# Optimization experiments

Hardware: AMD Instinct MI355X
Metric: run time of the kernel (lower is better)

## Reference

```python
import jax, jax.numpy as jnp
import numpy as np

B, O, I, D = 8, 128, 128, 1024


def setup_inputs() -> dict:
    key = jax.random.key(0)
    ks = jax.random.split(key, 10)
    s = 1.0 / np.sqrt(2 * D)  # torch Linear default-ish scale
    return {
        "output": jax.random.normal(ks[0], (B, O, D), jnp.float32),
        "context": jax.random.normal(ks[1], (B, I, D), jnp.float32),
        "mask": jax.random.randint(ks[2], (B, I), 0, 2, jnp.int32),
        # self.w = Linear(2*dim, dim), split into the output-half and context-half
        "w_out_w": jax.random.normal(ks[3], (D, D), jnp.float32) * s,
        "w_ctx_w": jax.random.normal(ks[4], (D, D), jnp.float32) * s,
        "w_b": jax.random.normal(ks[5], (D,), jnp.float32) * s,
        # self.score = Linear(dim, 1)
        "score_w": jax.random.normal(ks[6], (D,), jnp.float32) * (1.0 / np.sqrt(D)),
        "score_b": jnp.zeros((), jnp.float32),
        # self.linear_out = Linear(2*dim, dim)
        "lin_w": jax.random.normal(ks[7], (2 * D, D), jnp.float32) * s,
        "lin_b": jax.random.normal(ks[8], (D,), jnp.float32) * s,
    }


def reference(output, context, mask, w_out_w, w_ctx_w, w_b, score_w, score_b, lin_w, lin_b):
    # Additive (Bahdanau) attention.
    # cat(out, ctx) @ W^T == out @ W1 + ctx @ W2  -> avoid [B,O,I,2D] concat.
    s_out = jnp.einsum('bod,de->boe', output, w_out_w)            # [B,O,D]
    s_ctx = jnp.einsum('bid,de->bie', context, w_ctx_w)           # [B,I,D]
    h = jax.nn.leaky_relu(s_out[:, :, None, :] + s_ctx[:, None, :, :] + w_b)  # [B,O,I,D]
    score = jnp.einsum('boid,d->boi', h, score_w) + score_b       # [B,O,I]
    score = jnp.where(mask[:, None, :] == 1, -jnp.inf, score)
    attn = jax.nn.softmax(score, axis=-1)                         # [B,O,I]
    attn_output = jnp.einsum('boi,bid->bod', attn, context)       # mix=True: bmm
    # fn=True: linear_out on cat(attn_output, output) then leaky_relu
    combined = jnp.concatenate([attn_output, output], axis=-1)    # [B,O,2D]
    attn_output = jax.nn.leaky_relu(combined @ lin_w + lin_b)     # [B,O,D]
    return attn_output, attn
```

## Files before the change

### kernel.cpp

```cpp
#include <hip/hip_runtime.h>

namespace {

constexpr int kB = 8, kO = 128, kI = 128, kD = 1024;
constexpr long kOutAttnOff = (long)kB * kO * kD;

typedef __attribute__((ext_vector_type(8))) short short8;
typedef __attribute__((ext_vector_type(4))) float f32x4;

__device__ __forceinline__ float leaky(float x) { return fmaxf(x, 0.01f * x); }

__device__ __forceinline__ short f2bf(float f) {
    unsigned u = __builtin_bit_cast(unsigned, f);
    u += 0x7FFFu + ((u >> 16) & 1u);
    return (short)(u >> 16);
}

__device__ __forceinline__ void b8tof(const short8 v, float* f) {
    const unsigned* u = (const unsigned*)&v;
#pragma unroll
    for (int j = 0; j < 4; ++j) {
        f[2 * j]     = __builtin_bit_cast(float, u[j] << 16);
        f[2 * j + 1] = __builtin_bit_cast(float, u[j] & 0xffff0000u);
    }
}

__device__ __forceinline__ void gll16(const void* g, void* l) {
    __builtin_amdgcn_global_load_lds(
        (const __attribute__((address_space(1))) int*)g,
        (__attribute__((address_space(3))) int*)l, 16, 0, 0);
}

__global__ __launch_bounds__(256)
void conv_all(const float* __restrict__ output, const float* __restrict__ context,
              const float* __restrict__ w1, const float* __restrict__ w2,
              const float* __restrict__ lin,
              short* __restrict__ ob16, short* __restrict__ cb16,
              short* __restrict__ w1t, short* __restrict__ w2t,
              short* __restrict__ lint)
{
    __shared__ float T[64][68];
    const int bid = blockIdx.x, tid = threadIdx.x;

    if (bid < 1024) {
        const int idx = bid * 256 + tid;
        const float* src; short* dst; int i;
        if (idx < (1 << 17)) { src = output;  dst = ob16; i = idx; }
        else                 { src = context; dst = cb16; i = idx - (1 << 17); }
        const float4* s4 = (const float4*)src + (long)i * 2;
        const float4 v0 = s4[0], v1 = s4[1];
        short8 r;
        r[0] = f2bf(v0.x); r[1] = f2bf(v0.y); r[2] = f2bf(v0.z); r[3] = f2bf(v0.w);
        r[4] = f2bf(v1.x); r[5] = f2bf(v1.y); r[6] = f2bf(v1.z); r[7] = f2bf(v1.w);
        *(short8*)(dst + (long)i * 8) = r;
        return;
    }

    const int tb = bid - 1024;
    const float* src; short* dst; long C, R; int t2;
    if (tb < 256)      { src = w1;  dst = w1t;  R = 1024; C = 1024; t2 = tb; }
    else if (tb < 512) { src = w2;  dst = w2t;  R = 1024; C = 1024; t2 = tb - 256; }
    else               { src = lin; dst = lint; R = 2048; C = 1024; t2 = tb - 512; }
    const int tr = t2 >> 4, tc = t2 & 15;
    const int r = tid >> 2, q = tid & 3;

    const float* s = src + (long)(tr * 64 + r) * C + tc * 64 + q * 16;
    const float4 a0 = ((const float4*)s)[0];
    const float4 a1 = ((const float4*)s)[1];
    const float4 a2 = ((const float4*)s)[2];
    const float4 a3 = ((const float4*)s)[3];
    *(float4*)&T[r][q * 16 + 0]  = a0;
    *(float4*)&T[r][q * 16 + 4]  = a1;
    *(float4*)&T[r][q * 16 + 8]  = a2;
    *(float4*)&T[r][q * 16 + 12] = a3;
    __syncthreads();

    short8 o0, o1;
#pragma unroll
    for (int j = 0; j < 8; ++j)  o0[j] = f2bf(T[q * 16 + j][r]);
#pragma unroll
    for (int j = 0; j < 8; ++j)  o1[j] = f2bf(T[q * 16 + 8 + j][r]);
    short* dp = dst + (long)(tc * 64 + r) * R + tr * 64 + q * 16;
    *(short8*)dp       = o0;
    *((short8*)dp + 1) = o1;
}

__global__ __launch_bounds__(256)
void mm_jobs(const short* __restrict__ ob16, const short* __restrict__ cb16,
             const short* __restrict__ w1t, const short* __restrict__ w2t,
             const short* __restrict__ lint,
             const float* __restrict__ w_b, const float* __restrict__ lin_b,
             float* __restrict__ s_out, short* __restrict__ s_ctx16,
             float* __restrict__ outlin, short* __restrict__ ctxlin)
{
    __shared__ short As[2][64][64];
    __shared__ short Bs[2][128][64];
    const int tid = threadIdx.x;
    const int t = blockIdx.x;
    const int lane = tid & 63, w = tid >> 6;

    const short *Ap, *Bp;
    int lda, ldb, bm, bn, ldc;
    const float* bias = nullptr;
    float* Cf = nullptr;
    short* Ch = nullptr;

    if (t < 384) {
        const int job = t >> 7, jt = t & 127;
        bm = (jt >> 3) * 64; bn = (jt & 7) * 128;
        lda = 1024; ldc = 1024;
        if (job == 0)      { Ap = ob16; Bp = w1t;         ldb = 1024; bias = w_b;   Cf = s_out;   }
        else if (job == 1) { Ap = cb16; Bp = w2t;         ldb = 1024;               Ch = s_ctx16; }
        else               { Ap = ob16; Bp = lint + 1024; ldb = 2048; bias = lin_b; Cf = outlin;  }
    } else {
        const int tt = t - 384, bz = tt >> 4, tw = tt & 15;
        bm = tw * 64; bn = 0;
        Ap = lint; lda = 2048;
        Bp = cb16 + (long)bz * (kI * kD); ldb = 1024;
        Ch = ctxlin + (long)bz * (kD * kI); ldc = 128;
    }

    const int m0 = (w >> 1) * 32, n0 = (w & 1) * 64;
    const int fr = lane & 15, fcol = lane >> 4, sl = lane & 7;
    const int r8 = lane >> 3;
    const int sw8 = ((lane & 7) ^ r8) * 8;
    const int w16 = w * 16, w32 = w * 32;

    f32x4 acc[2][4] = {};

    auto stage = [&](int buf, int k0) {
        const short* ga = Ap + (long)(bm + w16 + r8) * lda + k0 + sw8;
        gll16(ga,                 &As[buf][w16][0]);
        gll16(ga + 8 * (long)lda, &As[buf][w16 + 8][0]);
        const short* gb = Bp + (long)(bn + w32 + r8) * ldb + k0 + sw8;
        gll16(gb,                  &Bs[buf][w32][0]);
        gll16(gb + 8 * (long)ldb,  &Bs[buf][w32 + 8][0]);
        gll16(gb + 16 * (long)ldb, &Bs[buf][w32 + 16][0]);
        gll16(gb + 24 * (long)ldb, &Bs[buf][w32 + 24][0]);
    };

    stage(0, 0);
    __syncthreads();
    int cur = 0;
    for (int s = 0; s < 16; ++s) {
        if (s < 15) stage(cur ^ 1, (s + 1) << 6);
#pragma unroll
        for (int ks8 = 0; ks8 < 8; ks8 += 4) {
            const int sa = ((ks8 + fcol) ^ sl) * 8;
            short8 a[2], b[4];
#pragma unroll
            for (int mi = 0; mi < 2; ++mi)
                a[mi] = *(const short8*)&As[cur][m0 + mi * 16 + fr][sa];
#pragma unroll
            for (int ni = 0; ni < 4; ++ni)
                b[ni] = *(const short8*)&Bs[cur][n0 + ni * 16 + fr][sa];
#pragma unroll
            for (int mi = 0; mi < 2; ++mi)
#pragma unroll
                for (int ni = 0; ni < 4; ++ni)
                    acc[mi][ni] = __builtin_amdgcn_mfma_f32_16x16x32_bf16(
                        a[mi], b[ni], acc[mi][ni], 0, 0, 0);
        }
        __syncthreads();
        cur ^= 1;
    }

    float bv[4] = {0, 0, 0, 0};
    if (bias) {
#pragma unroll
        for (int ni = 0; ni < 4; ++ni) bv[ni] = bias[bn + n0 + ni * 16 + fr];
    }
#pragma unroll
    for (int mi = 0; mi < 2; ++mi)
#pragma unroll
        for (int ni = 0; ni < 4; ++ni)
#pragma unroll
            for (int r = 0; r < 4; ++r) {
                const int row = bm + m0 + mi * 16 + ((lane >> 4) << 2) + r;
                const int col = bn + n0 + ni * 16 + fr;
                float v = acc[mi][ni][r] + bv[ni];
                if (Ch) Ch[(long)row * ldc + col] = f2bf(v);
                else    Cf[(long)row * ldc + col] = v;
            }
}

__global__ __launch_bounds__(256)
void score_final(const float* __restrict__ s_out, const short* __restrict__ s_ctx16,
                 const float* __restrict__ score_w, const float* __restrict__ score_b,
                 const int* __restrict__ mask, const short* __restrict__ ctxlin,
                 const float* __restrict__ outlin, float* __restrict__ out_main,
                 float* __restrict__ attn_f32)
{
    __shared__ float As[2][1032];
    __shared__ __align__(16) char CsPool[32768];
    __shared__ float Wsh[1024];
    __shared__ float Ps[4][2][128];
    __shared__ float Psi[4][128];
    __shared__ float so_sh[2];
    __shared__ int   Msk[128];
    __shared__ __align__(16) short Pl[16][136];

    short* CsS = (short*)CsPool;
    const int b   = blockIdx.x;
    const int o0  = blockIdx.y * 2;
    const int tid = threadIdx.x;
    const int wv  = tid >> 6;
    const int ln  = tid & 63;
    const int fr  = ln & 15, fg = ln >> 4;

    const float* arow = s_out + (long)(b * kO + o0) * kD;
#pragma unroll
    for (int q = 0; q < 2; ++q) {
        const int tq = tid + q * 256;
        const int rr = tq >> 8, c4 = (tq & 255) * 4;
        *(float4*)&As[rr][c4] = *(const float4*)&arow[(long)rr * kD + c4];
    }
    *(float4*)&Wsh[tid * 4] = *(const float4*)&score_w[tid * 4];
    if (tid < 128) Msk[tid] = mask[b * kI + tid];
    {
        short* pf = &Pl[0][0];
        for (int j = tid; j < 272; j += 256) *(short8*)(pf + j * 8) = short8{};
    }

    const short* crow = s_ctx16 + (long)b * kI * kD;
    auto stageCs = [&](int buf, int dc) {
#pragma unroll
        for (int it = 0; it < 4; ++it) {
            const int rb = wv * 32 + it * 8;
            const int r  = rb + (ln >> 3);
            const int sc = (ln & 7) ^ (r & 7);
            gll16(crow + (long)r * kD + dc + sc * 8, CsS + buf * 8192 + rb * 64);
        }
    };

    stageCs(0, 0);
    __syncthreads();

    if (wv < 2) {
        float acc = 0.0f;
#pragma unroll
        for (int j = 0; j < 16; j += 4) {
            const float4 av = *(const float4*)&As[wv][ln * 16 + j];
            const float4 ww = *(const float4*)&Wsh[ln * 16 + j];
            acc = fmaf(av.x, ww.x, acc); acc = fmaf(av.y, ww.y, acc);
            acc = fmaf(av.z, ww.z, acc); acc = fmaf(av.w, ww.w, acc);
        }
#pragma unroll
        for (int d = 1; d < 64; d <<= 1) acc += __shfl_xor(acc, d, 64);
        if (ln == 0) so_sh[wv] = acc;
    }

    float sa0[2] = {}, sa1[2] = {};
    float si0 = 0.0f, si1 = 0.0f;
    const int kb = wv * 16;

    int buf = 0;
    for (int c = 0; c < 16; ++c) {
        const int dc = c * 64;
        if (c < 15) stageCs(buf ^ 1, dc + 64);
        const int sc0 = ((wv * 2 + 0) ^ (ln & 7)) * 8;
        const int sc1 = ((wv * 2 + 1) ^ (ln & 7)) * 8;
        const short8 cA0 = *(const short8*)&CsS[buf * 8192 + ln * 64 + sc0];
        const short8 cA1 = *(const short8*)&CsS[buf * 8192 + ln * 64 + sc1];
        const short8 cB0 = *(const short8*)&CsS[buf * 8192 + (ln + 64) * 64 + sc0];
        const short8 cB1 = *(const short8*)&CsS[buf * 8192 + (ln + 64) * 64 + sc1];
        float c0[16], c1[16];
        b8tof(cA0, c0); b8tof(cA1, c0 + 8);
        b8tof(cB0, c1); b8tof(cB1, c1 + 8);
        float wr[16], av[2][16];
#pragma unroll
        for (int q = 0; q < 4; ++q) {
            *(float4*)&wr[q * 4]    = *(const float4*)&Wsh[dc + kb + q * 4];
            *(float4*)&av[0][q * 4] = *(const float4*)&As[0][dc + kb + q * 4];
            *(float4*)&av[1][q * 4] = *(const float4*)&As[1][dc + kb + q * 4];
        }
#pragma unroll
        for (int d = 0; d < 16; ++d) {
            si0 = fmaf(c0[d], wr[d], si0);
            si1 = fmaf(c1[d], wr[d], si1);
#pragma unroll
            for (int o = 0; o < 2; ++o) {
                sa0[o] = fmaf(__builtin_fabsf(av[o][d] + c0[d]), wr[d], sa0[o]);
                sa1[o] = fmaf(__builtin_fabsf(av[o][d] + c1[d]), wr[d], sa1[o]);
            }
        }
        __syncthreads();
        buf ^= 1;
    }

    short* Bsh = (short*)CsPool;
    const short* ctxb = ctxlin + (long)b * (kD * kI);
    auto stageB = [&](int half, int nc) {
#pragma unroll
        for (int it = 0; it < 4; ++it) {
            const int rb = wv * 16 + it * 4;
            const int r  = rb + (ln >> 4);
            const int n  = nc * 64 + r;
            const int sc = (ln & 15) ^ (r & 7);
            gll16(ctxb + (long)n * kI + sc * 8, Bsh + half * 8192 + rb * kI);
        }
    };
    stageB(0, 0);

#pragma unroll
    for (int o = 0; o < 2; ++o) {
        Ps[wv][o][ln]      = (o == 0) ? sa0[0] : sa0[1];
        Ps[wv][o][ln + 64] = (o == 0) ? sa1[0] : sa1[1];
    }
    Psi[wv][ln]      = si0;
    Psi[wv][ln + 64] = si1;
    __syncthreads();

    if (wv < 2) {
        const int ow = wv;
        const float negInf = -__builtin_huge_valf();
        const float sb = score_b[0];
        const float siT0 = Psi[0][ln] + Psi[1][ln] + Psi[2][ln] + Psi[3][ln];
        const float siT1 = Psi[0][ln + 64] + Psi[1][ln + 64]
                         + Psi[2][ln + 64] + Psi[3][ln + 64];
        const float saT0 = Ps[0][ow][ln] + Ps[1][ow][ln]
                         + Ps[2][ow][ln] + Ps[3][ow][ln];
        const float saT1 = Ps[0][ow][ln + 64] + Ps[1][ow][ln + 64]
                         + Ps[2][ow][ln + 64] + Ps[3][ow][ln + 64];
        const float soV = so_sh[ow];
        float s0 = 0.505f * (soV + siT0) + 0.495f * saT0 + sb;
        float s1 = 0.505f * (soV + siT1) + 0.495f * saT1 + sb;
        if (Msk[ln]      != 0) s0 = negInf;
        if (Msk[ln + 64] != 0) s1 = negInf;

        float m = fmaxf(s0, s1);
#pragma unroll
        for (int d = 1; d < 64; d <<= 1) m = fmaxf(m, __shfl_xor(m, d, 64));
        const float e0 = __expf(s0 - m);
        const float e1 = __expf(s1 - m);
        float sum = e0 + e1;
#pragma unroll
        for (int d = 1; d < 64; d <<= 1) sum += __shfl_xor(sum, d, 64);
        const float inv = 1.0f / sum;

        const long rowoff = (long)(b * kO + o0 + ow) * kI;
        const float p0 = e0 * inv, p1 = e1 * inv;
        attn_f32[rowoff + ln]      = p0;
        attn_f32[rowoff + ln + 64] = p1;
        Pl[ow][ln]      = f2bf(p0);
        Pl[ow][ln + 64] = f2bf(p1);
    }
    __syncthreads();

    int half = 0;
    for (int nc = 0; nc < 16; ++nc) {
        if (nc < 15) stageB(half ^ 1, nc + 1);
        const short* Bc = Bsh + half * 8192;
        f32x4 acc{};
#pragma unroll
        for (int ks = 0; ks < 4; ++ks) {
            const short8 a = *(const short8*)&Pl[fr][ks * 32 + fg * 8];
            const int sc = ((ks * 4 + fg) ^ (fr & 7)) * 8;
            const short8 bb = *(const short8*)&Bc[(wv * 16 + fr) * kI + sc];
            acc = __builtin_amdgcn_mfma_f32_16x16x32_bf16(a, bb, acc, 0, 0, 0);
        }
        if (fg == 0) {
#pragma unroll
            for (int r = 0; r < 2; ++r) {
                const int n = nc * 64 + wv * 16 + fr;
                const long off = (long)(b * kO + o0 + r) * kD + n;
                out_main[off] = leaky(acc[r] + outlin[off]);
            }
        }
        __syncthreads();
        half ^= 1;
    }
}

}

extern "C" void kernel_launch(void* const* d_in, const int* in_sizes, int n_in,
                              void* d_out, int out_size, void* d_ws, size_t ws_size,
                              hipStream_t stream)
{
    const float* output  = (const float*)d_in[0];
    const float* context = (const float*)d_in[1];
    const int*   mask    = (const int*)d_in[2];
    const float* w_out_w = (const float*)d_in[3];
    const float* w_ctx_w = (const float*)d_in[4];
    const float* w_b     = (const float*)d_in[5];
    const float* score_w = (const float*)d_in[6];
    const float* score_b = (const float*)d_in[7];
    const float* lin_w   = (const float*)d_in[8];
    const float* lin_b   = (const float*)d_in[9];

    float* out_main = (float*)d_out;
    float* out_attn = out_main + kOutAttnOff;
    float* s_out    = out_main;

    char* wp = (char*)d_ws;
    short* s_ctx16 = (short*)wp;  wp += (size_t)2 << 20;
    short* ob16    = (short*)wp;  wp += (size_t)2 << 20;
    short* cb16    = (short*)wp;  wp += (size_t)2 << 20;
    short* w1t     = (short*)wp;  wp += (size_t)2 << 20;
    short* w2t     = (short*)wp;  wp += (size_t)2 << 20;
    short* lint    = (short*)wp;  wp += (size_t)4 << 20;
    float* outlin  = (float*)wp;  wp += (size_t)4 << 20;
    short* ctxlin  = (short*)wp;

    const dim3 blk(256);

    hipLaunchKernelGGL(conv_all, dim3(2048), blk, 0, stream,
        output, context, w_out_w, w_ctx_w, lin_w, ob16, cb16, w1t, w2t, lint);

    hipLaunchKernelGGL(mm_jobs, dim3(512), blk, 0, stream,
        ob16, cb16, w1t, w2t, lint, w_b, lin_b, s_out, s_ctx16, outlin, ctxlin);

    hipLaunchKernelGGL(score_final, dim3(8, 64), blk, 0, stream,
        s_out, s_ctx16, score_w, score_b, mask, ctxlin, outlin, out_main, out_attn);
}
```

Before: 64.56 us.

## Triple-buffer LDS staging with explicit vmcnt waits in GEMM and score kernels

Replaces double-buffered global_load_lds staging with a three-slot ring in mm_jobs, the score loop and the final bmm loop of score_final. Two tiles are prefetched ahead, and the full __syncthreads is swapped for partial s_waitcnt vmcnt waits plus a raw s_barrier. The aim is to keep more global loads in flight and cut barrier and latency stalls between k-steps. In exchange it uses more LDS per block, which may lower occupancy. The hand-written vmcnt counts also depend on the exact order of other global memory operations in flight.

```diff
diff --git a/kernel.cpp b/kernel.cpp
--- a/kernel.cpp
+++ b/kernel.cpp
@@ -30,6 +30,12 @@
         (const __attribute__((address_space(1))) int*)g,
         (__attribute__((address_space(3))) int*)l, 16, 0, 0);
 }
+
+#define VMWAIT4() asm volatile("s_waitcnt vmcnt(4)" ::: "memory")
+#define VMWAIT6() asm volatile("s_waitcnt vmcnt(6)" ::: "memory")
+#define VMWAIT0() asm volatile("s_waitcnt vmcnt(0)" ::: "memory")
+#define LGKM0()   asm volatile("s_waitcnt lgkmcnt(0)" ::: "memory")
+#define BAR()     __builtin_amdgcn_s_barrier()
 
 __global__ __launch_bounds__(256)
 void conv_all(const float* __restrict__ output, const float* __restrict__ context,
@@ -93,8 +99,8 @@
              float* __restrict__ s_out, short* __restrict__ s_ctx16,
              float* __restrict__ outlin, short* __restrict__ ctxlin)
 {
-    __shared__ short As[2][64][64];
-    __shared__ short Bs[2][128][64];
+    __shared__ short As[3][64][64];
+    __shared__ short Bs[3][128][64];
     const int tid = threadIdx.x;
     const int t = blockIdx.x;
     const int lane = tid & 63, w = tid >> 6;
@@ -140,10 +146,13 @@
     };
 
     stage(0, 0);
-    __syncthreads();
-    int cur = 0;
+    stage(1, 64);
+    VMWAIT6();
+    BAR();
+
+    int cur = 0, s2 = 2;
     for (int s = 0; s < 16; ++s) {
-        if (s < 15) stage(cur ^ 1, (s + 1) << 6);
+        if (s + 2 < 16) stage(s2, (s + 2) << 6);
 #pragma unroll
         for (int ks8 = 0; ks8 < 8; ks8 += 4) {
             const int sa = ((ks8 + fcol) ^ sl) * 8;
@@ -161,8 +170,11 @@
                     acc[mi][ni] = __builtin_amdgcn_mfma_f32_16x16x32_bf16(
                         a[mi], b[ni], acc[mi][ni], 0, 0, 0);
         }
-        __syncthreads();
-        cur ^= 1;
+        if (s < 14)       VMWAIT6();
+        else if (s == 14) VMWAIT0();
+        if (s < 15) BAR();
+        cur = (cur == 2) ? 0 : cur + 1;
+        s2  = (s2 == 2) ? 0 : s2 + 1;
     }
 
     float bv[4] = {0, 0, 0, 0};
@@ -192,7 +204,7 @@
                  float* __restrict__ attn_f32)
 {
     __shared__ float As[2][1032];
-    __shared__ __align__(16) char CsPool[32768];
+    __shared__ __align__(16) char CsPool[49152];
     __shared__ float Wsh[1024];
     __shared__ float Ps[4][2][128];
     __shared__ float Psi[4][128];
@@ -208,6 +220,20 @@
     const int ln  = tid & 63;
     const int fr  = ln & 15, fg = ln >> 4;
 
+    const short* crow = s_ctx16 + (long)b * kI * kD;
+    auto stageCs = [&](int slot, int dc) {
+#pragma unroll
+        for (int it = 0; it < 4; ++it) {
+            const int rb = wv * 32 + it * 8;
+            const int r  = rb + (ln >> 3);
+            const int sc = (ln & 7) ^ (r & 7);
+            gll16(crow + (long)r * kD + dc + sc * 8, CsS + slot * 8192 + rb * 64);
+        }
+    };
+
+    stageCs(0, 0);
+    stageCs(1, 64);
+
     const float* arow = s_out + (long)(b * kO + o0) * kD;
 #pragma unroll
     for (int q = 0; q < 2; ++q) {
@@ -222,19 +248,9 @@
         for (int j = tid; j < 272; j += 256) *(short8*)(pf + j * 8) = short8{};
     }
 
-    const short* crow = s_ctx16 + (long)b * kI * kD;
-    auto stageCs = [&](int buf, int dc) {
-#pragma unroll
-        for (int it = 0; it < 4; ++it) {
-            const int rb = wv * 32 + it * 8;
-            const int r  = rb + (ln >> 3);
-            const int sc = (ln & 7) ^ (r & 7);
-            gll16(crow + (long)r * kD + dc + sc * 8, CsS + buf * 8192 + rb * 64);
-        }
-    };
-
-    stageCs(0, 0);
-    __syncthreads();
+    VMWAIT4();
+    LGKM0();
+    BAR();
 
     if (wv < 2) {
         float acc = 0.0f;
@@ -254,16 +270,17 @@
     float si0 = 0.0f, si1 = 0.0f;
     const int kb = wv * 16;
 
-    int buf = 0;
+    int buf = 0, s2 = 2;
     for (int c = 0; c < 16; ++c) {
+        if (c + 2 < 16) stageCs(s2, (c + 2) * 64);
         const int dc = c * 64;
-        if (c < 15) stageCs(buf ^ 1, dc + 64);
+        const short* Cb = CsS + buf * 8192;
         const int sc0 = ((wv * 2 + 0) ^ (ln & 7)) * 8;
         const int sc1 = ((wv * 2 + 1) ^ (ln & 7)) * 8;
-        const short8 cA0 = *(const short8*)&CsS[buf * 8192 + ln * 64 + sc0];
-        const short8 cA1 = *(const short8*)&CsS[buf * 8192 + ln * 64 + sc1];
-        const short8 cB0 = *(const short8*)&CsS[buf * 8192 + (ln + 64) * 64 + sc0];
-        const short8 cB1 = *(const short8*)&CsS[buf * 8192 + (ln + 64) * 64 + sc1];
+        const short8 cA0 = *(const short8*)&Cb[ln * 64 + sc0];
+        const short8 cA1 = *(const short8*)&Cb[ln * 64 + sc1];
+        const short8 cB0 = *(const short8*)&Cb[(ln + 64) * 64 + sc0];
+        const short8 cB1 = *(const short8*)&Cb[(ln + 64) * 64 + sc1];
         float c0[16], c1[16];
         b8tof(cA0, c0); b8tof(cA1, c0 + 8);
         b8tof(cB0, c1); b8tof(cB1, c1 + 8);
@@ -284,23 +301,27 @@
                 sa1[o] = fmaf(__builtin_fabsf(av[o][d] + c1[d]), wr[d], sa1[o]);
             }
         }
-        __syncthreads();
-        buf ^= 1;
+        if (c < 14)       VMWAIT4();
+        else if (c == 14) VMWAIT0();
+        BAR();
+        buf = (buf == 2) ? 0 : buf + 1;
+        s2  = (s2 == 2) ? 0 : s2 + 1;
     }
 
     short* Bsh = (short*)CsPool;
     const short* ctxb = ctxlin + (long)b * (kD * kI);
-    auto stageB = [&](int half, int nc) {
+    auto stageB = [&](int slot, int nc) {
 #pragma unroll
         for (int it = 0; it < 4; ++it) {
             const int rb = wv * 16 + it * 4;
             const int r  = rb + (ln >> 4);
             const int n  = nc * 64 + r;
             const int sc = (ln & 15) ^ (r & 7);
-            gll16(ctxb + (long)n * kI + sc * 8, Bsh + half * 8192 + rb * kI);
+            gll16(ctxb + (long)n * kI + sc * 8, Bsh + slot * 8192 + rb * kI);
         }
     };
     stageB(0, 0);
+    stageB(1, 1);
 
 #pragma unroll
     for (int o = 0; o < 2; ++o) {
@@ -309,7 +330,8 @@
     }
     Psi[wv][ln]      = si0;
     Psi[wv][ln + 64] = si1;
-    __syncthreads();
+    LGKM0();
+    BAR();
 
     if (wv < 2) {
         const int ow = wv;
@@ -345,12 +367,14 @@
         Pl[ow][ln]      = f2bf(p0);
         Pl[ow][ln + 64] = f2bf(p1);
     }
-    __syncthreads();
-
-    int half = 0;
+    VMWAIT4();
+    LGKM0();
+    BAR();
+
+    int h = 0, h2 = 2;
     for (int nc = 0; nc < 16; ++nc) {
-        if (nc < 15) stageB(half ^ 1, nc + 1);
-        const short* Bc = Bsh + half * 8192;
+        if (nc + 2 < 16) stageB(h2, nc + 2);
+        const short* Bc = Bsh + h * 8192;
         f32x4 acc{};
 #pragma unroll
         for (int ks = 0; ks < 4; ++ks) {
@@ -367,8 +391,11 @@
                 out_main[off] = leaky(acc[r] + outlin[off]);
             }
         }
-        __syncthreads();
-        half ^= 1;
+        if (nc < 14)       VMWAIT4();
+        else if (nc == 14) VMWAIT0();
+        if (nc < 15) BAR();
+        h  = (h == 2) ? 0 : h + 1;
+        h2 = (h2 == 2) ? 0 : h2 + 1;
     }
 }
 
```

After: 64.43 us. No clear change (-0.2%).
